# Optimization experiments

Measured on AMD Instinct MI355X. Metric: run time of the kernel, lower is better.

Reference implementation:

```python
import jax, jax.numpy as jnp
import numpy as np
import math

B, F, M, H, W, PD, KS = 2048, 512, 16, 32, 32, 64, 11
K = KS * KS
R = KS // 2
SIGMA = float(KS) / 3.0
HW = H * W


def _pos_encoding(gaze):
    # (B,2) -> (B,PD); interleaved sin/cos per axis
    half = PD // 2
    div = jnp.exp(jnp.arange(0, half, 2, dtype=jnp.float32) * -(math.log(10000.0) / half))  # (half/2,)
    def enc(p):  # p: (B,1)
        s = jnp.sin(p * div)
        c = jnp.cos(p * div)
        return jnp.stack([s, c], axis=-1).reshape(-1, half)
    return jnp.concatenate([enc(gaze[:, 0:1]), enc(gaze[:, 1:2])], axis=1)


def _adaptive_avg_pool3(x):
    # x: (B,C,H,W) -> (B,C,3,3), matching torch AdaptiveAvgPool2d(3)
    def bounds(n):
        return [(int(np.floor(i * n / 3)), int(np.ceil((i + 1) * n / 3))) for i in range(3)]
    hb, wb = bounds(x.shape[2]), bounds(x.shape[3])
    rows = []
    for (h0, h1) in hb:
        cols = [x[:, :, h0:h1, w0:w1].mean(axis=(2, 3)) for (w0, w1) in wb]
        rows.append(jnp.stack(cols, axis=-1))
    return jnp.stack(rows, axis=-2)  # (B,C,3,3)


def _conv(x, k, b):
    y = jax.lax.conv_general_dilated(x, k, (1, 1), 'SAME',
                                     dimension_numbers=('NCHW', 'OIHW', 'NCHW'))
    return y + b[None, :, None, None]


def setup_inputs() -> dict:
    key = jax.random.key(0)
    ks = jax.random.split(key, 20)
    n = lambda i, shp, sc=0.02: (jax.random.normal(ks[i], shp, dtype=jnp.float32) * sc)
    inp = {
        'features': jax.random.normal(ks[0], (B, F), dtype=jnp.float32),
        'cell_state': jax.random.normal(ks[1], (B, M, H, W), dtype=jnp.float32),
        'gaze_coords': jax.random.uniform(ks[2], (B, 2), dtype=jnp.float32),
        # input_gate: Linear(F+PD,256) -> ReLU -> Linear(256,128) -> ReLU
        'w1': n(3, (F + PD, 256)), 'b1': jnp.zeros((256,), jnp.float32),
        'w2': n(4, (256, 128)), 'b2': jnp.zeros((128,), jnp.float32),
        # write_value: Linear(128, M*K)
        'wv': n(5, (128, M * K)), 'bv': jnp.zeros((M * K,), jnp.float32),
        # strength_head: Linear(2M,64) -> ReLU -> Linear(64,1) -> Sigmoid
        'ws1': n(6, (2 * M, 64)), 'bs1': jnp.zeros((64,), jnp.float32),
        'ws2': n(7, (64, 1)), 'bs2': jnp.zeros((1,), jnp.float32),
        # output_gate convs + final linear
        'ck1': n(8, (128, M, 3, 3)), 'cb1': jnp.zeros((128,), jnp.float32),
        'ck2': n(9, (64, 128, 3, 3)), 'cb2': jnp.zeros((64,), jnp.float32),
        'wo': n(10, (64 * 9, 64 * 9)), 'bo': jnp.zeros((64 * 9,), jnp.float32),
    }
    return inp


def reference(features, cell_state, gaze_coords, w1, b1, w2, b2, wv, bv,
              ws1, bs1, ws2, bs2, ck1, cb1, ck2, cb2, wo, bo):
    # --- input gate + write values ---
    pe = _pos_encoding(gaze_coords)
    g = jax.nn.relu(jnp.concatenate([features, pe], axis=1) @ w1 + b1)
    g = jax.nn.relu(g @ w2 + b2)
    write_vals = (g @ wv + bv).reshape(B, K, M)

    # --- neighborhood geometry ---
    offs = jnp.arange(-R, R + 1)
    ox, oy = jnp.meshgrid(offs, offs, indexing='xy')
    ox, oy = ox.reshape(-1), oy.reshape(-1)  # (K,)
    gx = jnp.clip(gaze_coords[:, 0] * (W - 1), 0.0, W - 1.0)
    gy = jnp.clip(gaze_coords[:, 1] * (H - 1), 0.0, H - 1.0)
    x0 = jnp.floor(gx).astype(jnp.int32)
    y0 = jnp.floor(gy).astype(jnp.int32)
    xs = jnp.clip(x0[:, None] + ox[None, :], 0, W - 1)  # (B,K)
    ys = jnp.clip(y0[:, None] + oy[None, :], 0, H - 1)
    dx = xs.astype(jnp.float32) - gx[:, None]
    dy = ys.astype(jnp.float32) - gy[:, None]
    gauss = jnp.exp(-(dx * dx + dy * dy) / max(1e-6, 2.0 * SIGMA ** 2))
    nw = gauss / jnp.maximum(gauss.sum(axis=1, keepdims=True), 1e-8)  # (B,K)

    # --- gather previous values ---
    idx = ys * W + xs  # (B,K) flat indices
    cell_flat = cell_state.reshape(B, M, HW)
    prev = jnp.take_along_axis(cell_flat, idx[:, None, :], axis=2).transpose(0, 2, 1)  # (B,K,M)

    # --- learned per-cell strength gate ---
    gate_in = jnp.concatenate([prev, write_vals], axis=-1)  # (B,K,2M)
    s = jax.nn.relu(gate_in @ ws1 + bs1)
    gstr = jax.nn.sigmoid(s @ ws2 + bs2)  # (B,K,1)
    w_all = nw[:, :, None] * gstr  # (B,K,1)
    new_vals = (1.0 - w_all) * prev + w_all * write_vals  # (B,K,M)

    # --- weighted scatter-add with normalization ---
    b_idx = jnp.arange(B)[:, None]
    den = jnp.zeros((B, HW), jnp.float32).at[b_idx, idx].add(w_all[..., 0])
    num = jnp.zeros((B, HW, M), jnp.float32).at[b_idx, idx].add(w_all * new_vals)
    keep = 1.0 - jnp.minimum(den, 1.0)  # (B,HW)
    updated_flat = keep[:, None, :] * cell_flat + num.transpose(0, 2, 1)
    updated = updated_flat.reshape(B, M, H, W)

    # --- output gate ---
    y = jax.nn.relu(_conv(updated, ck1, cb1))
    y = jax.nn.relu(_conv(y, ck2, cb2))
    y = _adaptive_avg_pool3(y).reshape(B, -1)  # (B,576)
    out = y @ wo + bo
    return out, updated
```

## Files before the change

kernel.cpp:

```cpp
#include <hip/hip_runtime.h>
#include <hip/hip_bf16.h>
#include <math.h>

#define NB 2048
#define NF 512
#define NM 16
#define NK 121
#define NMK 1936

typedef __attribute__((ext_vector_type(8))) short bf16x8;
typedef __attribute__((ext_vector_type(4))) float f32x4;

#define MFMA __builtin_amdgcn_mfma_f32_16x16x32_bf16

static __device__ __forceinline__ unsigned short f2b(float f) {
  unsigned int u = __float_as_uint(f);
  unsigned int lsb = (u >> 16) & 1u;
  u += 0x7fffu + lsb;
  return (unsigned short)(u >> 16);
}

static __device__ __forceinline__ unsigned cvtpk(float lo, float hi) {
  unsigned r;
  asm("v_cvt_pk_bf16_f32 %0, %1, %2" : "=v"(r) : "v"(lo), "v"(hi));
  return r;
}

__global__ __launch_bounds__(256) void k_pack(
    const float* __restrict__ ck1, const float* __restrict__ ck2,
    unsigned short* __restrict__ ap1, unsigned short* __restrict__ ap2) {
  int i = blockIdx.x * 256 + threadIdx.x;
  if (i < 20480) {
    int j = i & 7, lane = (i >> 3) & 63;
    int m2 = (i >> 9) & 1, kc = (i >> 10) % 5, w = i / 5120;
    int c1 = w * 32 + m2 * 16 + (lane & 15);
    int k = kc * 32 + ((lane >> 4) << 3) + j;
    int s = k >> 4, ci = k & 15;
    float v = 0.f;
    if (s < 9) v = ck1[((c1 * 16 + ci) * 3 + s / 3) * 3 + (s % 3)];
    ap1[i] = f2b(v);
  }
  int i2 = i - 20480;
  if (i2 >= 0 && i2 < 73728) {
    int j = i2 & 7, lane = (i2 >> 3) & 63;
    int kc = (i2 >> 9) & 3, s = (i2 >> 11) % 9, mt = i2 / 18432;
    int c2 = mt * 16 + (lane & 15);
    int c1 = kc * 32 + ((lane >> 4) << 3) + j;
    float v = ck2[((c2 * 128 + c1) * 3 + s / 3) * 3 + (s % 3)];
    ap2[i2] = f2b(v);
  }
}

__global__ __launch_bounds__(256) void k_mlp(
    const float* __restrict__ feat, const float* __restrict__ gaze,
    const float* __restrict__ w1, const float* __restrict__ b1,
    const float* __restrict__ w2, const float* __restrict__ b2,
    const float* __restrict__ wv, const float* __restrict__ bv,
    float* __restrict__ wvout) {
  __shared__ float xs[4][576];
  __shared__ float g1[4][256];
  __shared__ float g2[4][128];
  const int t = threadIdx.x;
  const int b0 = blockIdx.x * 4;

  for (int e = t; e < 4 * 512; e += 256) {
    int r = e >> 9, i = e & 511;
    xs[r][i] = feat[(size_t)(b0 + r) * NF + i];
  }
  if (t < 4 * 64) {
    int r = t >> 6, i = t & 63;
    int axis = i >> 5;
    int ii = i & 31;
    int jj = ii >> 1;
    int isc = ii & 1;
    float p = gaze[(size_t)(b0 + r) * 2 + axis];
    float dv = expf(-(float)(2 * jj) * 0.28782313662425575f);
    float ang = p * dv;
    xs[r][512 + i] = isc ? cosf(ang) : sinf(ang);
  }
  __syncthreads();
  {
    float acc[4];
    float bb = b1[t];
#pragma unroll
    for (int r = 0; r < 4; r++) acc[r] = bb;
#pragma unroll 8
    for (int i = 0; i < 576; i++) {
      float w = w1[(size_t)i * 256 + t];
#pragma unroll
      for (int r = 0; r < 4; r++) acc[r] = fmaf(xs[r][i], w, acc[r]);
    }
#pragma unroll
    for (int r = 0; r < 4; r++) g1[r][t] = fmaxf(acc[r], 0.f);
  }
  __syncthreads();
  if (t < 128) {
    float acc[4];
    float bb = b2[t];
#pragma unroll
    for (int r = 0; r < 4; r++) acc[r] = bb;
#pragma unroll 8
    for (int i = 0; i < 256; i++) {
      float w = w2[(size_t)i * 128 + t];
#pragma unroll
      for (int r = 0; r < 4; r++) acc[r] = fmaf(g1[r][i], w, acc[r]);
    }
#pragma unroll
    for (int r = 0; r < 4; r++) g2[r][t] = fmaxf(acc[r], 0.f);
  }
  __syncthreads();
  {
    float acc7[7][4];
    float accT[4];
#pragma unroll
    for (int jj = 0; jj < 7; jj++) {
      float bb = bv[t + 256 * jj];
#pragma unroll
      for (int r = 0; r < 4; r++) acc7[jj][r] = bb;
    }
    {
      float bb = (t < 144) ? bv[1792 + t] : 0.f;
#pragma unroll
      for (int r = 0; r < 4; r++) accT[r] = bb;
    }
#pragma unroll 2
    for (int i = 0; i < 128; i++) {
      float g[4];
#pragma unroll
      for (int r = 0; r < 4; r++) g[r] = g2[r][i];
      const float* wrow = wv + (size_t)i * NMK;
#pragma unroll
      for (int jj = 0; jj < 7; jj++) {
        float w = wrow[t + 256 * jj];
#pragma unroll
        for (int r = 0; r < 4; r++) acc7[jj][r] = fmaf(g[r], w, acc7[jj][r]);
      }
      if (t < 144) {
        float w = wrow[1792 + t];
#pragma unroll
        for (int r = 0; r < 4; r++) accT[r] = fmaf(g[r], w, accT[r]);
      }
    }
#pragma unroll
    for (int r = 0; r < 4; r++) {
      float* orow = wvout + (size_t)(b0 + r) * NMK;
#pragma unroll
      for (int jj = 0; jj < 7; jj++) orow[t + 256 * jj] = acc7[jj][r];
      if (t < 144) orow[1792 + t] = accT[r];
    }
  }
}

__global__ __launch_bounds__(256) void k_update(
    const float* __restrict__ cell, const float* __restrict__ gaze,
    const float* __restrict__ wvin,
    const float* __restrict__ ws1, const float* __restrict__ bs1,
    const float* __restrict__ ws2, const float* __restrict__ bs2,
    float* __restrict__ updated, unsigned short* __restrict__ ubf) {
  __shared__ float numl[16][129];
  __shared__ float denl[128];
  __shared__ float ws1s[2048];
  __shared__ float bs1s[64];
  __shared__ float ws2s[64];
  __shared__ float nws[121];
  __shared__ float z2part[2][128];
  __shared__ float gsum_s;
  __shared__ float bs2s;
  const int t = threadIdx.x;
  const int b = blockIdx.x;
  const int kk = t & 127;
  const int hf = t >> 7;

  for (int e = t; e < 16 * 129; e += 256) ((float*)numl)[e] = 0.f;
  if (t < 128) denl[t] = 0.f;
  for (int e = t; e < 2048; e += 256) ws1s[e] = ws1[e];
  if (t < 64) { bs1s[t] = bs1[t]; ws2s[t] = ws2[t]; }
  if (t == 0) bs2s = bs2[0];

  const float gx = fminf(fmaxf(gaze[(size_t)b * 2 + 0] * 31.f, 0.f), 31.f);
  const float gy = fminf(fmaxf(gaze[(size_t)b * 2 + 1] * 31.f, 0.f), 31.f);
  const int x0 = (int)floorf(gx);
  const int y0 = (int)floorf(gy);
  const int wx0 = max(0, x0 - 5);
  const int wy0 = max(0, y0 - 5);

  int xi = 0, yi = 0;
  if (kk < NK) {
    int ox = kk % 11 - 5;
    int oy = kk / 11 - 5;
    xi = min(max(x0 + ox, 0), 31);
    yi = min(max(y0 + oy, 0), 31);
    if (hf == 0) {
      float dx = (float)xi - gx, dy = (float)yi - gy;
      nws[kk] = expf(-(dx * dx + dy * dy) * (9.0f / 242.0f));
    }
  }
  __syncthreads();
  if (t < 64) {
    float s = nws[t] + ((t + 64 < NK) ? nws[t + 64] : 0.f);
    s += __shfl_xor(s, 1, 64);
    s += __shfl_xor(s, 2, 64);
    s += __shfl_xor(s, 4, 64);
    s += __shfl_xor(s, 8, 64);
    s += __shfl_xor(s, 16, 64);
    s += __shfl_xor(s, 32, 64);
    if (t == 0) gsum_s = fmaxf(s, 1e-8f);
  }
  __syncthreads();

  float prev[16], wvv[16];
  if (kk < NK) {
    const int idx = yi * 32 + xi;
#pragma unroll
    for (int m = 0; m < 16; m++) prev[m] = cell[(size_t)b * 16384 + m * 1024 + idx];
#pragma unroll
    for (int m = 0; m < 16; m++) wvv[m] = wvin[(size_t)b * NMK + kk * 16 + m];
    float z2p = 0.f;
    const int j0 = hf * 32;
#pragma unroll 4
    for (int j = j0; j < j0 + 32; j++) {
      float z = bs1s[j];
#pragma unroll
      for (int i = 0; i < 16; i++) z = fmaf(prev[i], ws1s[i * 64 + j], z);
#pragma unroll
      for (int i = 0; i < 16; i++) z = fmaf(wvv[i], ws1s[(16 + i) * 64 + j], z);
      z = fmaxf(z, 0.f);
      z2p = fmaf(z, ws2s[j], z2p);
    }
    z2part[hf][kk] = z2p;
  }
  __syncthreads();

  if (t < NK) {
    const float nw = nws[t] / gsum_s;
    const int local = (yi - wy0) * 11 + (xi - wx0);
    float z2 = bs2s + z2part[0][t] + z2part[1][t];
    float gstr = 1.f / (1.f + expf(-z2));
    float w = nw * gstr;
    atomicAdd(&denl[local], w);
#pragma unroll
    for (int m = 0; m < 16; m++) {
      float nv = (1.f - w) * prev[m] + w * wvv[m];
      atomicAdd(&numl[m][local], w * nv);
    }
  }
  __syncthreads();

  const size_t cb = (size_t)b * 16384;

  {
    const int hw4 = t * 4;
    const int yy = hw4 >> 5, xx0 = hw4 & 31;
    const int wy = yy - wy0;
    float kp[4];
    int loc[4];
    bool inw[4];
#pragma unroll
    for (int c = 0; c < 4; ++c) {
      int wx = xx0 + c - wx0;
      bool in = ((unsigned)wy < 11u) && ((unsigned)wx < 11u);
      inw[c] = in;
      loc[c] = in ? wy * 11 + wx : 0;
      kp[c] = in ? 1.f - fminf(denl[loc[c]], 1.f) : 1.f;
    }
#pragma unroll 4
    for (int m = 0; m < 16; ++m) {
      float4 cv = *(const float4*)&cell[cb + m * 1024 + hw4];
      float4 ov;
      ov.x = kp[0] * cv.x + (inw[0] ? numl[m][loc[0]] : 0.f);
      ov.y = kp[1] * cv.y + (inw[1] ? numl[m][loc[1]] : 0.f);
      ov.z = kp[2] * cv.z + (inw[2] ? numl[m][loc[2]] : 0.f);
      ov.w = kp[3] * cv.w + (inw[3] ? numl[m][loc[3]] : 0.f);
      *(float4*)&updated[cb + m * 1024 + hw4] = ov;
    }
  }

  unsigned* ub32 = (unsigned*)ubf + (size_t)b * 9248;
  {
    const int p2 = t & 3;
    const int c0 = p2 * 4;
    const int hwb = t >> 2;
#pragma unroll 4
    for (int it = 0; it < 16; ++it) {
      const int hw = hwb + it * 64;
      const int yy = hw >> 5, xx = hw & 31;
      const int wy = yy - wy0, wx = xx - wx0;
      const bool in = ((unsigned)wy < 11u) && ((unsigned)wx < 11u);
      const int loc = in ? wy * 11 + wx : 0;
      const float kp = in ? 1.f - fminf(denl[loc], 1.f) : 1.f;
      float v0 = kp * cell[cb + (c0 + 0) * 1024 + hw] + (in ? numl[c0 + 0][loc] : 0.f);
      float v1 = kp * cell[cb + (c0 + 1) * 1024 + hw] + (in ? numl[c0 + 1][loc] : 0.f);
      float v2 = kp * cell[cb + (c0 + 2) * 1024 + hw] + (in ? numl[c0 + 2][loc] : 0.f);
      float v3 = kp * cell[cb + (c0 + 3) * 1024 + hw] + (in ? numl[c0 + 3][loc] : 0.f);
      uint2 pk;
      pk.x = cvtpk(v0, v1);
      pk.y = cvtpk(v2, v3);
      *(uint2*)(ub32 + ((size_t)((yy + 1) * 34 + (xx + 1)) * 8 + p2 * 2)) = pk;
    }
  }

  for (int e = t; e < 1056; e += 256) {
    int j = e & 7, pos = e >> 3;
    int row, col;
    if (pos < 34)       { row = 0;             col = pos; }
    else if (pos < 68)  { row = 33;            col = pos - 34; }
    else if (pos < 100) { row = pos - 68 + 1;  col = 0; }
    else                { row = pos - 100 + 1; col = 33; }
    ub32[(row * 34 + col) * 8 + j] = 0u;
  }
}

#define Y1ROW 4488
__global__ __launch_bounds__(256, 2) void k_conv3(
    const unsigned short* __restrict__ ubf,
    const unsigned short* __restrict__ ap1, const float* __restrict__ cb1,
    const unsigned short* __restrict__ ap2, const float* __restrict__ cb2,
    float* __restrict__ ypool) {
  __shared__ unsigned short y1[6][33][136];
  const int t = threadIdx.x;
  const int b = blockIdx.x;
  const int lane = t & 63;
  const int w = t >> 6;
  const int ln = lane & 15;
  const int q = lane >> 4;
  const int qh = q >> 1, ql = q & 1;

  const unsigned short* ubb = ubf + (size_t)b * 18496;
  const unsigned short* ap2w = ap2 + (size_t)(w * 36 * 64 + lane) * 8;
  const unsigned short* ap1w = ap1 + (size_t)(w * 10 * 64 + lane) * 8;

  f32x4 cb2r;
  {
    int c2b = w * 16 + q * 4;
    cb2r = f32x4{cb2[c2b], cb2[c2b + 1], cb2[c2b + 2], cb2[c2b + 3]};
  }
  f32x4 cb1r[2];
#pragma unroll
  for (int m2 = 0; m2 < 2; m2++) {
    int c1b = w * 32 + m2 * 16 + q * 4;
    cb1r[m2] = f32x4{cb1[c1b], cb1[c1b + 1], cb1[c1b + 2], cb1[c1b + 3]};
  }

  int po1[5];
#pragma unroll
  for (int kc = 0; kc < 5; kc++) {
    int s = 2 * kc + qh;
    if (s > 8) s = 0;
    po1[kc] = (s / 3) * 544 + (s % 3) * 16;
  }

  for (int e = t; e < 6 * 68; e += 256) {
    int s = e / 68, wd = e % 68;
    ((unsigned*)y1)[s * (Y1ROW / 2) + wd] = 0u;
  }

  f32x4 PL0 = {0.f, 0.f, 0.f, 0.f}, PL1 = PL0, PL2 = PL0;
  f32x4 PH0 = PL0, PH1 = PL0, PH2 = PL0;

#pragma unroll 1
  for (int ti = 0; ti < 8; ti++) {
    const int r0 = ti * 4;

    const unsigned short* p1 = ap1w;
    const unsigned short* p2 = ap2w;
    asm volatile("" : "+v"(p1), "+v"(p2));

    bf16x8 a1[5][2];
#pragma unroll
    for (int kc = 0; kc < 5; kc++)
#pragma unroll
      for (int m2 = 0; m2 < 2; m2++)
        a1[kc][m2] = *(const bf16x8*)(p1 + (size_t)((kc * 2 + m2) * 64) * 8);

    const int nrow = (ti == 0) ? 6 : 4;
    const int abase = (ti == 0) ? -1 : r0 + 1;
#pragma unroll 2
    for (int nt = 0; nt < nrow * 2; nt++) {
      const int ry = nt >> 1, h = nt & 1;
      const int gy1 = abase + ry;
      const int slot = (gy1 + 1) % 6;
      const int gyc = min(max(gy1, 0), 31);
      const int x = h * 16 + ln;
      const unsigned short* bp = ubb + gyc * 544 + x * 16 + ql * 8;
      bf16x8 f0 = *(const bf16x8*)(bp + po1[0]);
      bf16x8 f1 = *(const bf16x8*)(bp + po1[1]);
      bf16x8 f2 = *(const bf16x8*)(bp + po1[2]);
      bf16x8 f3 = *(const bf16x8*)(bp + po1[3]);
      bf16x8 f4 = *(const bf16x8*)(bp + po1[4]);
      f32x4 acc0 = cb1r[0], acc1 = cb1r[1];
      acc0 = MFMA(a1[0][0], f0, acc0, 0, 0, 0); acc1 = MFMA(a1[0][1], f0, acc1, 0, 0, 0);
      acc0 = MFMA(a1[1][0], f1, acc0, 0, 0, 0); acc1 = MFMA(a1[1][1], f1, acc1, 0, 0, 0);
      acc0 = MFMA(a1[2][0], f2, acc0, 0, 0, 0); acc1 = MFMA(a1[2][1], f2, acc1, 0, 0, 0);
      acc0 = MFMA(a1[3][0], f3, acc0, 0, 0, 0); acc1 = MFMA(a1[3][1], f3, acc1, 0, 0, 0);
      acc0 = MFMA(a1[4][0], f4, acc0, 0, 0, 0); acc1 = MFMA(a1[4][1], f4, acc1, 0, 0, 0);
      const bool inr = ((unsigned)gy1 < 32u);
#pragma unroll
      for (int m2 = 0; m2 < 2; m2++) {
        f32x4 a = m2 ? acc1 : acc0;
        float v0 = inr ? fmaxf(a[0], 0.f) : 0.f;
        float v1 = inr ? fmaxf(a[1], 0.f) : 0.f;
        float v2 = inr ? fmaxf(a[2], 0.f) : 0.f;
        float v3 = inr ? fmaxf(a[3], 0.f) : 0.f;
        uint2 pk;
        pk.x = cvtpk(v0, v1);
        pk.y = cvtpk(v2, v3);
        *(uint2*)&y1[slot][1 + x][w * 32 + m2 * 16 + q * 4] = pk;
      }
    }

    bf16x8 a2[9][4];
#pragma unroll
    for (int s = 0; s < 9; s++)
#pragma unroll
      for (int kc = 0; kc < 4; kc++)
        a2[s][kc] = *(const bf16x8*)(p2 + (size_t)((s * 4 + kc) * 64) * 8);

    __syncthreads();

    int rowoff[6];
    {
      int s0 = (r0) % 6;
#pragma unroll
      for (int yr = 0; yr < 6; yr++) {
        int s = s0 + yr;
        if (s >= 6) s -= 6;
        rowoff[yr] = s * Y1ROW;
      }
    }
    __builtin_amdgcn_s_setprio(1);
#pragma unroll
    for (int h = 0; h < 2; h++) {
      const int xg = h * 16 + ln;
      const unsigned short* rp[6];
#pragma unroll
      for (int yr = 0; yr < 6; yr++) rp[yr] = &y1[0][0][0] + rowoff[yr] + q * 8;
      int pco[3];
#pragma unroll
      for (int dx = 0; dx < 3; dx++) {
        int pc = xg + dx;
        if (pc == 33) pc = 0;
        pco[dx] = pc * 136;
      }
      f32x4 A0 = cb2r, A1 = cb2r, A2 = cb2r, A3 = cb2r;
#pragma unroll
      for (int yr = 0; yr < 6; yr++)
#pragma unroll
        for (int kc = 0; kc < 4; kc++)
#pragma unroll
          for (int dx = 0; dx < 3; dx++) {
            bf16x8 fr = *(const bf16x8*)(rp[yr] + pco[dx] + kc * 32);
#pragma unroll
            for (int dy = 0; dy < 3; dy++) {
              const int rr = yr - dy;
              if (rr < 0 || rr > 3) continue;
              f32x4& ac = (rr == 0) ? A0 : ((rr == 1) ? A1 : ((rr == 2) ? A2 : A3));
              ac = MFMA(a2[dy * 3 + dx][kc], fr, ac, 0, 0, 0);
            }
          }
#pragma unroll
      for (int rr = 0; rr < 4; rr++) {
        const int grow = r0 + rr;
        const float rm0 = (grow <= 10) ? 1.f : 0.f;
        const float rm1 = (grow >= 10 && grow <= 21) ? 1.f : 0.f;
        const float rm2 = (grow >= 21) ? 1.f : 0.f;
        f32x4 v = (rr == 0) ? A0 : ((rr == 1) ? A1 : ((rr == 2) ? A2 : A3));
        v[0] = fmaxf(v[0], 0.f);
        v[1] = fmaxf(v[1], 0.f);
        v[2] = fmaxf(v[2], 0.f);
        v[3] = fmaxf(v[3], 0.f);
        if (h == 0) {
          PL0 += v * rm0; PL1 += v * rm1; PL2 += v * rm2;
        } else {
          PH0 += v * rm0; PH1 += v * rm1; PH2 += v * rm2;
        }
      }
    }
    __builtin_amdgcn_s_setprio(0);
    __syncthreads();
  }

  const float mA0 = (ln <= 10) ? 1.f : 0.f;
  const float mA1 = (ln >= 10) ? 1.f : 0.f;
  const float mB1 = (ln <= 5) ? 1.f : 0.f;
  const float mB2 = (ln >= 5) ? 1.f : 0.f;
  f32x4 t00 = PL0 * mA0, t01 = PL0 * mA1 + PH0 * mB1, t02 = PH0 * mB2;
  f32x4 t10 = PL1 * mA0, t11 = PL1 * mA1 + PH1 * mB1, t12 = PH1 * mB2;
  f32x4 t20 = PL2 * mA0, t21 = PL2 * mA1 + PH2 * mB1, t22 = PH2 * mB2;

  {
    f32x4* tv[9] = {&t00, &t01, &t02, &t10, &t11, &t12, &t20, &t21, &t22};
#pragma unroll
    for (int i = 0; i < 9; i++) {
      f32x4& v = *tv[i];
#pragma unroll
      for (int c = 0; c < 4; c++) {
        float s = v[c];
        s += __shfl_xor(s, 1, 64);
        s += __shfl_xor(s, 2, 64);
        s += __shfl_xor(s, 4, 64);
        s += __shfl_xor(s, 8, 64);
        v[c] = s;
      }
    }
  }

  float* yp = ypool + (size_t)b * 576 + (w * 16 + q * 4) * 9;
#define PWRITE(tv, ph, pw)                                                      \
  if (ln == (ph * 3 + pw)) {                                                    \
    const float dv = 1.f / (float)(((ph == 1) ? 12 : 11) * ((pw == 1) ? 12 : 11)); \
    yp[0 * 9 + ph * 3 + pw] = tv[0] * dv;                                       \
    yp[1 * 9 + ph * 3 + pw] = tv[1] * dv;                                       \
    yp[2 * 9 + ph * 3 + pw] = tv[2] * dv;                                       \
    yp[3 * 9 + ph * 3 + pw] = tv[3] * dv;                                       \
  }
  PWRITE(t00, 0, 0) PWRITE(t01, 0, 1) PWRITE(t02, 0, 2)
  PWRITE(t10, 1, 0) PWRITE(t11, 1, 1) PWRITE(t12, 1, 2)
  PWRITE(t20, 2, 0) PWRITE(t21, 2, 1) PWRITE(t22, 2, 2)
#undef PWRITE
}

__global__ __launch_bounds__(256) void k_out(
    const float* __restrict__ ypool, const float* __restrict__ wo,
    const float* __restrict__ bo, float* __restrict__ out) {
  __shared__ float ys[4][576];
  const int t = threadIdx.x;
  const int b0 = blockIdx.x * 4;
  for (int e = t; e < 4 * 576; e += 256) {
    int r = e / 576, i = e % 576;
    ys[r][i] = ypool[(size_t)(b0 + r) * 576 + i];
  }
  __syncthreads();
  float a0[4], a1[4], aT[4];
  {
    float bb0 = bo[t], bb1 = bo[t + 256];
    float bbT = (t < 64) ? bo[512 + t] : 0.f;
#pragma unroll
    for (int r = 0; r < 4; r++) { a0[r] = bb0; a1[r] = bb1; aT[r] = bbT; }
  }
#pragma unroll 2
  for (int i = 0; i < 576; i++) {
    const float* wr = wo + (size_t)i * 576;
    float w0 = wr[t], w1 = wr[t + 256];
    float g[4];
#pragma unroll
    for (int r = 0; r < 4; r++) g[r] = ys[r][i];
#pragma unroll
    for (int r = 0; r < 4; r++) {
      a0[r] = fmaf(g[r], w0, a0[r]);
      a1[r] = fmaf(g[r], w1, a1[r]);
    }
    if (t < 64) {
      float wT = wr[512 + t];
#pragma unroll
      for (int r = 0; r < 4; r++) aT[r] = fmaf(g[r], wT, aT[r]);
    }
  }
#pragma unroll
  for (int r = 0; r < 4; r++) {
    float* orow = out + (size_t)(b0 + r) * 576;
    orow[t] = a0[r];
    orow[t + 256] = a1[r];
    if (t < 64) orow[512 + t] = aT[r];
  }
}

extern "C" void kernel_launch(void* const* d_in, const int* in_sizes, int n_in,
                              void* d_out, int out_size, void* d_ws, size_t ws_size,
                              hipStream_t stream) {
  (void)in_sizes; (void)n_in; (void)out_size;
  const float* feat = (const float*)d_in[0];
  const float* cell = (const float*)d_in[1];
  const float* gaze = (const float*)d_in[2];
  const float* w1   = (const float*)d_in[3];
  const float* b1   = (const float*)d_in[4];
  const float* w2   = (const float*)d_in[5];
  const float* b2   = (const float*)d_in[6];
  const float* wv   = (const float*)d_in[7];
  const float* bv   = (const float*)d_in[8];
  const float* ws1  = (const float*)d_in[9];
  const float* bs1  = (const float*)d_in[10];
  const float* ws2  = (const float*)d_in[11];
  const float* bs2  = (const float*)d_in[12];
  const float* ck1  = (const float*)d_in[13];
  const float* cb1  = (const float*)d_in[14];
  const float* ck2  = (const float*)d_in[15];
  const float* cb2  = (const float*)d_in[16];
  const float* wo   = (const float*)d_in[17];
  const float* bo   = (const float*)d_in[18];

  float* out0    = (float*)d_out;
  float* updated = out0 + (size_t)NB * 576;
  float* wvout   = (float*)d_ws;
  float* ypool   = wvout + (size_t)NB * NMK;
  unsigned short* ap1 = (unsigned short*)(ypool + (size_t)NB * 576);
  unsigned short* ap2 = ap1 + 20480;
  unsigned short* ubf = ap2 + 73728;

  const size_t fixed_bytes = ((size_t)NB * (NMK + 576)) * 4 + (size_t)94208 * 2;
  const size_t wsz = ws_size ? ws_size : ((size_t)1 << 30);
  int chunk = 2048;
  while (chunk > 128 && fixed_bytes + (size_t)chunk * 36992 > wsz) chunk >>= 1;

  k_pack<<<dim3(368), dim3(256), 0, stream>>>(ck1, ck2, ap1, ap2);
  k_mlp<<<dim3(NB / 4), dim3(256), 0, stream>>>(feat, gaze, w1, b1, w2, b2, wv, bv, wvout);
  for (int b0 = 0; b0 < NB; b0 += chunk) {
    const int n = (NB - b0 < chunk) ? (NB - b0) : chunk;
    k_update<<<dim3(n), dim3(256), 0, stream>>>(
        cell + (size_t)b0 * 16384, gaze + (size_t)b0 * 2,
        wvout + (size_t)b0 * NMK, ws1, bs1, ws2, bs2,
        updated + (size_t)b0 * 16384, ubf);
    k_conv3<<<dim3(n), dim3(256), 0, stream>>>(
        ubf, ap1, cb1, ap2, cb2, ypool + (size_t)b0 * 576);
  }
  k_out<<<dim3(NB / 8 * 2), dim3(256), 0, stream>>>(ypool, wo, bo, out0);
}
```

Baseline: 1.106 ms.

## Fuse scatter-update and conv kernels into one per-batch kernel with shared LDS

Merges k_update and k_conv3 into a single kernel. It aliases the update-phase shared buffers onto the conv's y1 LDS region and drops the chunked launch loop. Each block writes its padded bf16 tile and then runs the convs on it after a barrier, which removes one launch per chunk and the gap between the two kernels. The bf16 tile still goes through global memory and is read back by the same block soon after, so it may hit in cache. In exchange, the update phase now runs under launch_bounds(256,2) and the larger LDS footprint, which may limit occupancy, and the ws_size chunking safeguard is dropped.

```diff
diff --git a/kernel.cpp b/kernel.cpp
--- a/kernel.cpp
+++ b/kernel.cpp
@@ -151,174 +151,174 @@
   }
 }
 
-__global__ __launch_bounds__(256) void k_update(
+#define Y1ROW 4488
+__global__ __launch_bounds__(256, 2) void k_fused(
     const float* __restrict__ cell, const float* __restrict__ gaze,
     const float* __restrict__ wvin,
     const float* __restrict__ ws1, const float* __restrict__ bs1,
     const float* __restrict__ ws2, const float* __restrict__ bs2,
-    float* __restrict__ updated, unsigned short* __restrict__ ubf) {
-  __shared__ float numl[16][129];
-  __shared__ float denl[128];
-  __shared__ float ws1s[2048];
-  __shared__ float bs1s[64];
-  __shared__ float ws2s[64];
-  __shared__ float nws[121];
-  __shared__ float z2part[2][128];
-  __shared__ float gsum_s;
-  __shared__ float bs2s;
-  const int t = threadIdx.x;
-  const int b = blockIdx.x;
-  const int kk = t & 127;
-  const int hf = t >> 7;
-
-  for (int e = t; e < 16 * 129; e += 256) ((float*)numl)[e] = 0.f;
-  if (t < 128) denl[t] = 0.f;
-  for (int e = t; e < 2048; e += 256) ws1s[e] = ws1[e];
-  if (t < 64) { bs1s[t] = bs1[t]; ws2s[t] = ws2[t]; }
-  if (t == 0) bs2s = bs2[0];
-
-  const float gx = fminf(fmaxf(gaze[(size_t)b * 2 + 0] * 31.f, 0.f), 31.f);
-  const float gy = fminf(fmaxf(gaze[(size_t)b * 2 + 1] * 31.f, 0.f), 31.f);
-  const int x0 = (int)floorf(gx);
-  const int y0 = (int)floorf(gy);
-  const int wx0 = max(0, x0 - 5);
-  const int wy0 = max(0, y0 - 5);
-
-  int xi = 0, yi = 0;
-  if (kk < NK) {
-    int ox = kk % 11 - 5;
-    int oy = kk / 11 - 5;
-    xi = min(max(x0 + ox, 0), 31);
-    yi = min(max(y0 + oy, 0), 31);
-    if (hf == 0) {
-      float dx = (float)xi - gx, dy = (float)yi - gy;
-      nws[kk] = expf(-(dx * dx + dy * dy) * (9.0f / 242.0f));
-    }
-  }
-  __syncthreads();
-  if (t < 64) {
-    float s = nws[t] + ((t + 64 < NK) ? nws[t + 64] : 0.f);
-    s += __shfl_xor(s, 1, 64);
-    s += __shfl_xor(s, 2, 64);
-    s += __shfl_xor(s, 4, 64);
-    s += __shfl_xor(s, 8, 64);
-    s += __shfl_xor(s, 16, 64);
-    s += __shfl_xor(s, 32, 64);
-    if (t == 0) gsum_s = fmaxf(s, 1e-8f);
-  }
-  __syncthreads();
-
-  float prev[16], wvv[16];
-  if (kk < NK) {
-    const int idx = yi * 32 + xi;
-#pragma unroll
-    for (int m = 0; m < 16; m++) prev[m] = cell[(size_t)b * 16384 + m * 1024 + idx];
-#pragma unroll
-    for (int m = 0; m < 16; m++) wvv[m] = wvin[(size_t)b * NMK + kk * 16 + m];
-    float z2p = 0.f;
-    const int j0 = hf * 32;
-#pragma unroll 4
-    for (int j = j0; j < j0 + 32; j++) {
-      float z = bs1s[j];
-#pragma unroll
-      for (int i = 0; i < 16; i++) z = fmaf(prev[i], ws1s[i * 64 + j], z);
-#pragma unroll
-      for (int i = 0; i < 16; i++) z = fmaf(wvv[i], ws1s[(16 + i) * 64 + j], z);
-      z = fmaxf(z, 0.f);
-      z2p = fmaf(z, ws2s[j], z2p);
-    }
-    z2part[hf][kk] = z2p;
-  }
-  __syncthreads();
-
-  if (t < NK) {
-    const float nw = nws[t] / gsum_s;
-    const int local = (yi - wy0) * 11 + (xi - wx0);
-    float z2 = bs2s + z2part[0][t] + z2part[1][t];
-    float gstr = 1.f / (1.f + expf(-z2));
-    float w = nw * gstr;
-    atomicAdd(&denl[local], w);
-#pragma unroll
-    for (int m = 0; m < 16; m++) {
-      float nv = (1.f - w) * prev[m] + w * wvv[m];
-      atomicAdd(&numl[m][local], w * nv);
-    }
-  }
-  __syncthreads();
-
-  const size_t cb = (size_t)b * 16384;
-
-  {
-    const int hw4 = t * 4;
-    const int yy = hw4 >> 5, xx0 = hw4 & 31;
-    const int wy = yy - wy0;
-    float kp[4];
-    int loc[4];
-    bool inw[4];
-#pragma unroll
-    for (int c = 0; c < 4; ++c) {
-      int wx = xx0 + c - wx0;
-      bool in = ((unsigned)wy < 11u) && ((unsigned)wx < 11u);
-      inw[c] = in;
-      loc[c] = in ? wy * 11 + wx : 0;
-      kp[c] = in ? 1.f - fminf(denl[loc[c]], 1.f) : 1.f;
-    }
-#pragma unroll 4
-    for (int m = 0; m < 16; ++m) {
-      float4 cv = *(const float4*)&cell[cb + m * 1024 + hw4];
-      float4 ov;
-      ov.x = kp[0] * cv.x + (inw[0] ? numl[m][loc[0]] : 0.f);
-      ov.y = kp[1] * cv.y + (inw[1] ? numl[m][loc[1]] : 0.f);
-      ov.z = kp[2] * cv.z + (inw[2] ? numl[m][loc[2]] : 0.f);
-      ov.w = kp[3] * cv.w + (inw[3] ? numl[m][loc[3]] : 0.f);
-      *(float4*)&updated[cb + m * 1024 + hw4] = ov;
-    }
-  }
-
-  unsigned* ub32 = (unsigned*)ubf + (size_t)b * 9248;
-  {
-    const int p2 = t & 3;
-    const int c0 = p2 * 4;
-    const int hwb = t >> 2;
-#pragma unroll 4
-    for (int it = 0; it < 16; ++it) {
-      const int hw = hwb + it * 64;
-      const int yy = hw >> 5, xx = hw & 31;
-      const int wy = yy - wy0, wx = xx - wx0;
-      const bool in = ((unsigned)wy < 11u) && ((unsigned)wx < 11u);
-      const int loc = in ? wy * 11 + wx : 0;
-      const float kp = in ? 1.f - fminf(denl[loc], 1.f) : 1.f;
-      float v0 = kp * cell[cb + (c0 + 0) * 1024 + hw] + (in ? numl[c0 + 0][loc] : 0.f);
-      float v1 = kp * cell[cb + (c0 + 1) * 1024 + hw] + (in ? numl[c0 + 1][loc] : 0.f);
-      float v2 = kp * cell[cb + (c0 + 2) * 1024 + hw] + (in ? numl[c0 + 2][loc] : 0.f);
-      float v3 = kp * cell[cb + (c0 + 3) * 1024 + hw] + (in ? numl[c0 + 3][loc] : 0.f);
-      uint2 pk;
-      pk.x = cvtpk(v0, v1);
-      pk.y = cvtpk(v2, v3);
-      *(uint2*)(ub32 + ((size_t)((yy + 1) * 34 + (xx + 1)) * 8 + p2 * 2)) = pk;
-    }
-  }
-
-  for (int e = t; e < 1056; e += 256) {
-    int j = e & 7, pos = e >> 3;
-    int row, col;
-    if (pos < 34)       { row = 0;             col = pos; }
-    else if (pos < 68)  { row = 33;            col = pos - 34; }
-    else if (pos < 100) { row = pos - 68 + 1;  col = 0; }
-    else                { row = pos - 100 + 1; col = 33; }
-    ub32[(row * 34 + col) * 8 + j] = 0u;
-  }
-}
-
-#define Y1ROW 4488
-__global__ __launch_bounds__(256, 2) void k_conv3(
-    const unsigned short* __restrict__ ubf,
+    float* __restrict__ updated, unsigned short* __restrict__ ubf,
     const unsigned short* __restrict__ ap1, const float* __restrict__ cb1,
     const unsigned short* __restrict__ ap2, const float* __restrict__ cb2,
     float* __restrict__ ypool) {
-  __shared__ unsigned short y1[6][33][136];
+  __shared__ __align__(16) char smem[53856];
+  unsigned short (*y1)[33][136] = (unsigned short (*)[33][136])smem;
+  float* numl   = (float*)smem;
+  float* denl   = (float*)(smem + 8256);
+  float* ws1s   = (float*)(smem + 8768);
+  float* bs1s   = (float*)(smem + 16960);
+  float* ws2s   = (float*)(smem + 17216);
+  float* nwsS   = (float*)(smem + 17472);
+  float* z2part = (float*)(smem + 17956);
+  float* gsum_p = (float*)(smem + 18980);
+  float* bs2_p  = (float*)(smem + 18984);
+
   const int t = threadIdx.x;
   const int b = blockIdx.x;
+
+  {
+    const int kk = t & 127;
+    const int hf = t >> 7;
+
+    for (int e = t; e < 16 * 129; e += 256) numl[e] = 0.f;
+    if (t < 128) denl[t] = 0.f;
+    for (int e = t; e < 2048; e += 256) ws1s[e] = ws1[e];
+    if (t < 64) { bs1s[t] = bs1[t]; ws2s[t] = ws2[t]; }
+    if (t == 0) *bs2_p = bs2[0];
+
+    const float gx = fminf(fmaxf(gaze[(size_t)b * 2 + 0] * 31.f, 0.f), 31.f);
+    const float gy = fminf(fmaxf(gaze[(size_t)b * 2 + 1] * 31.f, 0.f), 31.f);
+    const int x0 = (int)floorf(gx);
+    const int y0 = (int)floorf(gy);
+    const int wx0 = max(0, x0 - 5);
+    const int wy0 = max(0, y0 - 5);
+
+    int xi = 0, yi = 0;
+    if (kk < NK) {
+      int ox = kk % 11 - 5;
+      int oy = kk / 11 - 5;
+      xi = min(max(x0 + ox, 0), 31);
+      yi = min(max(y0 + oy, 0), 31);
+      if (hf == 0) {
+        float dx = (float)xi - gx, dy = (float)yi - gy;
+        nwsS[kk] = expf(-(dx * dx + dy * dy) * (9.0f / 242.0f));
+      }
+    }
+    __syncthreads();
+    if (t < 64) {
+      float s = nwsS[t] + ((t + 64 < NK) ? nwsS[t + 64] : 0.f);
+      s += __shfl_xor(s, 1, 64);
+      s += __shfl_xor(s, 2, 64);
+      s += __shfl_xor(s, 4, 64);
+      s += __shfl_xor(s, 8, 64);
+      s += __shfl_xor(s, 16, 64);
+      s += __shfl_xor(s, 32, 64);
+      if (t == 0) *gsum_p = fmaxf(s, 1e-8f);
+    }
+    __syncthreads();
+
+    float prev[16], wvv[16];
+    if (kk < NK) {
+      const int idx = yi * 32 + xi;
+#pragma unroll
+      for (int m = 0; m < 16; m++) prev[m] = cell[(size_t)b * 16384 + m * 1024 + idx];
+#pragma unroll
+      for (int m = 0; m < 16; m++) wvv[m] = wvin[(size_t)b * NMK + kk * 16 + m];
+      float z2p = 0.f;
+      const int j0 = hf * 32;
+#pragma unroll 4
+      for (int j = j0; j < j0 + 32; j++) {
+        float z = bs1s[j];
+#pragma unroll
+        for (int i = 0; i < 16; i++) z = fmaf(prev[i], ws1s[i * 64 + j], z);
+#pragma unroll
+        for (int i = 0; i < 16; i++) z = fmaf(wvv[i], ws1s[(16 + i) * 64 + j], z);
+        z = fmaxf(z, 0.f);
+        z2p = fmaf(z, ws2s[j], z2p);
+      }
+      z2part[hf * 128 + kk] = z2p;
+    }
+    __syncthreads();
+
+    if (t < NK) {
+      const float nw = nwsS[t] / *gsum_p;
+      const int local = (yi - wy0) * 11 + (xi - wx0);
+      float z2 = *bs2_p + z2part[t] + z2part[128 + t];
+      float gstr = 1.f / (1.f + expf(-z2));
+      float w = nw * gstr;
+      atomicAdd(&denl[local], w);
+#pragma unroll
+      for (int m = 0; m < 16; m++) {
+        float nv = (1.f - w) * prev[m] + w * wvv[m];
+        atomicAdd(&numl[m * 129 + local], w * nv);
+      }
+    }
+    __syncthreads();
+
+    const size_t cb = (size_t)b * 16384;
+
+    {
+      const int hw4 = t * 4;
+      const int yy = hw4 >> 5, xx0 = hw4 & 31;
+      const int wy = yy - wy0;
+      float kp[4];
+      int loc[4];
+      bool inw[4];
+#pragma unroll
+      for (int c = 0; c < 4; ++c) {
+        int wx = xx0 + c - wx0;
+        bool in = ((unsigned)wy < 11u) && ((unsigned)wx < 11u);
+        inw[c] = in;
+        loc[c] = in ? wy * 11 + wx : 0;
+        kp[c] = in ? 1.f - fminf(denl[loc[c]], 1.f) : 1.f;
+      }
+#pragma unroll 4
+      for (int m = 0; m < 16; ++m) {
+        float4 cv = *(const float4*)&cell[cb + m * 1024 + hw4];
+        float4 ov;
+        ov.x = kp[0] * cv.x + (inw[0] ? numl[m * 129 + loc[0]] : 0.f);
+        ov.y = kp[1] * cv.y + (inw[1] ? numl[m * 129 + loc[1]] : 0.f);
+        ov.z = kp[2] * cv.z + (inw[2] ? numl[m * 129 + loc[2]] : 0.f);
+        ov.w = kp[3] * cv.w + (inw[3] ? numl[m * 129 + loc[3]] : 0.f);
+        *(float4*)&updated[cb + m * 1024 + hw4] = ov;
+      }
+    }
+
+    unsigned* ub32 = (unsigned*)ubf + (size_t)b * 9248;
+    {
+      const int p2 = t & 3;
+      const int c0 = p2 * 4;
+      const int hwb = t >> 2;
+#pragma unroll 4
+      for (int it = 0; it < 16; ++it) {
+        const int hw = hwb + it * 64;
+        const int yy = hw >> 5, xx = hw & 31;
+        const int wy = yy - wy0, wx = xx - wx0;
+        const bool in = ((unsigned)wy < 11u) && ((unsigned)wx < 11u);
+        const int loc = in ? wy * 11 + wx : 0;
+        const float kp = in ? 1.f - fminf(denl[loc], 1.f) : 1.f;
+        float v0 = kp * cell[cb + (c0 + 0) * 1024 + hw] + (in ? numl[(c0 + 0) * 129 + loc] : 0.f);
+        float v1 = kp * cell[cb + (c0 + 1) * 1024 + hw] + (in ? numl[(c0 + 1) * 129 + loc] : 0.f);
+        float v2 = kp * cell[cb + (c0 + 2) * 1024 + hw] + (in ? numl[(c0 + 2) * 129 + loc] : 0.f);
+        float v3 = kp * cell[cb + (c0 + 3) * 1024 + hw] + (in ? numl[(c0 + 3) * 129 + loc] : 0.f);
+        uint2 pk;
+        pk.x = cvtpk(v0, v1);
+        pk.y = cvtpk(v2, v3);
+        *(uint2*)(ub32 + ((size_t)((yy + 1) * 34 + (xx + 1)) * 8 + p2 * 2)) = pk;
+      }
+    }
+    for (int e = t; e < 1056; e += 256) {
+      int j = e & 7, pos = e >> 3;
+      int row, col;
+      if (pos < 34)       { row = 0;             col = pos; }
+      else if (pos < 68)  { row = 33;            col = pos - 34; }
+      else if (pos < 100) { row = pos - 68 + 1;  col = 0; }
+      else                { row = pos - 100 + 1; col = 33; }
+      ub32[(row * 34 + col) * 8 + j] = 0u;
+    }
+  }
+  __syncthreads();
+
   const int lane = t & 63;
   const int w = t >> 6;
   const int ln = lane & 15;
@@ -567,7 +567,7 @@
 extern "C" void kernel_launch(void* const* d_in, const int* in_sizes, int n_in,
                               void* d_out, int out_size, void* d_ws, size_t ws_size,
                               hipStream_t stream) {
-  (void)in_sizes; (void)n_in; (void)out_size;
+  (void)in_sizes; (void)n_in; (void)out_size; (void)ws_size;
   const float* feat = (const float*)d_in[0];
   const float* cell = (const float*)d_in[1];
   const float* gaze = (const float*)d_in[2];
@@ -596,21 +596,10 @@
   unsigned short* ap2 = ap1 + 20480;
   unsigned short* ubf = ap2 + 73728;
 
-  const size_t fixed_bytes = ((size_t)NB * (NMK + 576)) * 4 + (size_t)94208 * 2;
-  const size_t wsz = ws_size ? ws_size : ((size_t)1 << 30);
-  int chunk = 2048;
-  while (chunk > 128 && fixed_bytes + (size_t)chunk * 36992 > wsz) chunk >>= 1;
-
   k_pack<<<dim3(368), dim3(256), 0, stream>>>(ck1, ck2, ap1, ap2);
   k_mlp<<<dim3(NB / 4), dim3(256), 0, stream>>>(feat, gaze, w1, b1, w2, b2, wv, bv, wvout);
-  for (int b0 = 0; b0 < NB; b0 += chunk) {
-    const int n = (NB - b0 < chunk) ? (NB - b0) : chunk;
-    k_update<<<dim3(n), dim3(256), 0, stream>>>(
-        cell + (size_t)b0 * 16384, gaze + (size_t)b0 * 2,
-        wvout + (size_t)b0 * NMK, ws1, bs1, ws2, bs2,
-        updated + (size_t)b0 * 16384, ubf);
-    k_conv3<<<dim3(n), dim3(256), 0, stream>>>(
-        ubf, ap1, cb1, ap2, cb2, ypool + (size_t)b0 * 576);
-  }
+  k_fused<<<dim3(NB), dim3(256), 0, stream>>>(
+      cell, gaze, wvout, ws1, bs1, ws2, bs2, updated, ubf,
+      ap1, cb1, ap2, cb2, ypool);
   k_out<<<dim3(NB / 8 * 2), dim3(256), 0, stream>>>(ypool, wo, bo, out0);
 }
```

Result: slower. 1.172 ms (+6.0%).
